# Performance work log

Measured on AMD Instinct MI355X. Metric: run time of the kernel, lower is better.

## Reference

```python
import jax, jax.numpy as jnp
import numpy as np

N = 50000        # nodes
E = 1600000      # edges
D_IN = 128       # input feature size
H = 4            # attention heads
C = 16           # hidden_size1 (per-head out channels)
HC = H * C       # 64
HS2 = 64         # hidden_size2
EDGE_DIM = 4
EPS = 1e-5


def setup_inputs() -> dict:
    key = jax.random.key(0)
    ks = jax.random.split(key, 64)
    inp = {}
    inp["data_x"] = jax.random.normal(ks[0], (N, D_IN), jnp.float32)
    inp["data_edge_index"] = jax.random.randint(ks[1], (2, E), 0, N)
    inp["data_edge_attr"] = jax.random.normal(ks[2], (E, EDGE_DIM), jnp.float32)
    i = 3
    s = 0.1
    for l, din in enumerate([D_IN, HC]):
        inp[f"Wl{l}"] = jax.random.normal(ks[i], (din, HC), jnp.float32) * s; i += 1
        inp[f"bl{l}"] = jnp.zeros((HC,), jnp.float32)
        inp[f"Wr{l}"] = jax.random.normal(ks[i], (din, HC), jnp.float32) * s; i += 1
        inp[f"br{l}"] = jnp.zeros((HC,), jnp.float32)
        inp[f"We{l}"] = jax.random.normal(ks[i], (EDGE_DIM, HC), jnp.float32) * s; i += 1
        inp[f"att{l}"] = jax.random.normal(ks[i], (H, C), jnp.float32) * s; i += 1
        inp[f"bias{l}"] = jnp.zeros((HC,), jnp.float32)
        inp[f"g{l}"] = jnp.ones((HC,), jnp.float32)
        inp[f"be{l}"] = jnp.zeros((HC,), jnp.float32)
    inp["W1"] = jax.random.normal(ks[i], (HC, HS2), jnp.float32) * s; i += 1
    inp["b1"] = jnp.zeros((HS2,), jnp.float32)
    inp["gf"] = jnp.ones((HS2,), jnp.float32)
    inp["bf"] = jnp.zeros((HS2,), jnp.float32)
    inp["W2"] = jax.random.normal(ks[i], (HS2, 1), jnp.float32) * s; i += 1
    inp["b2"] = jnp.zeros((1,), jnp.float32)
    return inp


def batch_norm(x, g, b):
    mu = x.mean(0)
    var = x.var(0)  # biased variance, matching torch BN normalization
    return (x - mu) * jax.lax.rsqrt(var + EPS) * g + b


def gatv2_layer(x, src, dst, eattr, Wl, bl, Wr, br, We, att, bias):
    # GATv2Conv, add_self_loops=False, concat=True, negative_slope=0.2
    n = x.shape[0]
    xl = (x @ Wl + bl).reshape(n, H, C)   # source transform (x_j side)
    xr = (x @ Wr + br).reshape(n, H, C)   # destination transform (x_i side)
    e = (eattr @ We).reshape(-1, H, C)    # edge-feature transform
    m = xl[src] + xr[dst] + e             # [E,H,C]
    m = jnp.where(m > 0, m, 0.2 * m)      # LeakyReLU(0.2)
    a = jnp.einsum('ehc,hc->eh', m, att)  # attention logits [E,H]
    amax = jax.ops.segment_max(a, dst, num_segments=n)   # per-dst max
    a = jnp.exp(a - amax[dst])
    asum = jax.ops.segment_sum(a, dst, num_segments=n)
    alpha = a / (asum[dst] + 1e-16)       # per-destination softmax
    out = jax.ops.segment_sum(xl[src] * alpha[:, :, None], dst, num_segments=n)
    return out.reshape(n, HC) + bias


def reference(data_x, data_edge_index, data_edge_attr,
              Wl0, bl0, Wr0, br0, We0, att0, bias0, g0, be0,
              Wl1, bl1, Wr1, br1, We1, att1, bias1, g1, be1,
              W1, b1, gf, bf, W2, b2):
    src = data_edge_index[0]
    dst = data_edge_index[1]
    layers = [(Wl0, bl0, Wr0, br0, We0, att0, bias0, g0, be0),
              (Wl1, bl1, Wr1, br1, We1, att1, bias1, g1, be1)]
    x = data_x
    for (Wl, bl, Wr, br, We, att, bias, g, be) in layers:
        x = gatv2_layer(x, src, dst, data_edge_attr, Wl, bl, Wr, br, We, att, bias)
        x = jax.nn.elu(batch_norm(x, g, be))
    x = x @ W1 + b1
    x = jax.nn.elu(batch_norm(x, gf, bf))
    return 5.0 * jnp.tanh(x @ W2 + b2)
```

## Files before the change

### kernel.cpp

```cpp
#include <hip/hip_runtime.h>
#include <hip/hip_bf16.h>
#include <cmath>

#define HC 64
typedef __hip_bfloat16 bf16;
typedef unsigned int uint;
typedef float v4f __attribute__((ext_vector_type(4)));

__device__ __forceinline__ uint pack_bf2(float a, float b) {
    __hip_bfloat162 h = __float22bfloat162_rn(make_float2(a, b));
    return *reinterpret_cast<uint*>(&h);
}
__device__ __forceinline__ float bfl(uint u) { return __uint_as_float(u << 16); }
__device__ __forceinline__ float bfh(uint u) { return __uint_as_float(u & 0xffff0000u); }


__global__ __launch_bounds__(512) void bucket_hist_k(const int* __restrict__ dst,
                                                     int* __restrict__ bcnt, int E, int nbk) {
    __shared__ int lh[512];
    int t = threadIdx.x;
    for (int i = t; i < nbk; i += 512) lh[i] = 0;
    __syncthreads();
    int base = blockIdx.x * 8192;
#pragma unroll
    for (int k = 0; k < 16; ++k) {
        int e = base + k * 512 + t;
        if (e < E) atomicAdd(&lh[dst[e] >> 7], 1);
    }
    __syncthreads();
    for (int i = t; i < nbk; i += 512) if (lh[i]) atomicAdd(&bcnt[i], lh[i]);
}


__global__ __launch_bounds__(512) void bucket_scan_k(const int* __restrict__ bcnt,
                                                     int* __restrict__ bstart,
                                                     int* __restrict__ bcur, int nbk, int E) {
    __shared__ int tmp[512];
    int t = threadIdx.x;
    int v = (t < nbk) ? bcnt[t] : 0;
    tmp[t] = v;
    __syncthreads();
    for (int off = 1; off < 512; off <<= 1) {
        int a = (t >= off) ? tmp[t - off] : 0;
        __syncthreads();
        tmp[t] += a;
        __syncthreads();
    }
    if (t < nbk) { int ex = tmp[t] - v; bstart[t] = ex; bcur[t] = ex; }
    if (t == 0) bstart[nbk] = E;
}


__global__ __launch_bounds__(1024) void bucketA_k(
        const int* __restrict__ src, const int* __restrict__ dst,
        const float4* __restrict__ eattr, int* __restrict__ bcur,
        uint* __restrict__ tsd, uint2* __restrict__ tea, int E, int nbk) {
    __shared__ int lcnt[512];
    __shared__ int lbase[512];
    int t = threadIdx.x;
    for (int i = t; i < nbk; i += 1024) lcnt[i] = 0;
    __syncthreads();
    int base = blockIdx.x * 8192;
    int myb[8], mylp[8];
#pragma unroll
    for (int k = 0; k < 8; ++k) {
        int e = base + k * 1024 + t;
        if (e < E) {
            int b = dst[e] >> 7;
            myb[k] = b;
            mylp[k] = atomicAdd(&lcnt[b], 1);
        } else myb[k] = -1;
    }
    __syncthreads();
    for (int i = t; i < nbk; i += 1024) {
        int cc = lcnt[i];
        lbase[i] = cc ? atomicAdd(&bcur[i], cc) : 0;
    }
    __syncthreads();
#pragma unroll
    for (int k = 0; k < 8; ++k) {
        int e = base + k * 1024 + t;
        if (e >= E) continue;
        int pos = lbase[myb[k]] + mylp[k];
        int d = dst[e];
        tsd[pos] = (uint)src[e] | ((uint)(d & 127) << 25);
        float4 ea = eattr[e];
        tea[pos] = make_uint2(pack_bf2(ea.x, ea.y), pack_bf2(ea.z, ea.w));
    }
}


__global__ __launch_bounds__(256) void bucket_sort_k(
        const uint* __restrict__ tsd, const uint2* __restrict__ tea,
        const int* __restrict__ bstart,
        uint* __restrict__ spre_sorted, uint2* __restrict__ eat_sorted,
        int* __restrict__ row_start, int n) {
    __shared__ int cnt[128], pfx[128], cur[128];
    int b = blockIdx.x, t = threadIdx.x;
    int i0 = bstart[b], i1 = bstart[b + 1];
    int node0 = b << 7;
    if (t < 128) cnt[t] = 0;
    __syncthreads();
    for (int i = i0 + t; i < i1; i += 256) atomicAdd(&cnt[tsd[i] >> 25], 1);
    __syncthreads();
    if (t < 128) pfx[t] = cnt[t];
    __syncthreads();
    for (int off = 1; off < 128; off <<= 1) {
        int a = (t < 128 && t >= off) ? pfx[t - off] : 0;
        __syncthreads();
        if (t < 128) pfx[t] += a;
        __syncthreads();
    }
    if (t < 128) {
        int ex = pfx[t] - cnt[t];
        cur[t] = ex;
        if (node0 + t <= n) row_start[node0 + t] = i0 + ex;
    }
    __syncthreads();
    for (int i = i0 + t; i < i1; i += 256) {
        uint u = tsd[i];
        int dl = (int)(u >> 25);
        int pos = i0 + atomicAdd(&cur[dl], 1);
        spre_sorted[pos] = (u & 0x1FFFFFFu) << 7;
        eat_sorted[pos] = tea[i];
    }
}


__global__ __launch_bounds__(256) void lin128_k(
        const float* __restrict__ x, int n,
        const float* __restrict__ Wl, const float* __restrict__ bl,
        const float* __restrict__ Wr, const float* __restrict__ br,
        bf16* __restrict__ xl, bf16* __restrict__ xr, int ngroups16) {
    __shared__ uint sWl2[64 * 64];
    __shared__ uint sWr2[64 * 64];
    __shared__ float sx[16 * 128];
    int t = threadIdx.x;
    for (int i = t; i < 64 * 64; i += 256) {
        int k2 = i >> 6, c = i & 63;
        sWl2[i] = pack_bf2(Wl[(2 * k2) * 64 + c], Wl[(2 * k2 + 1) * 64 + c]);
        sWr2[i] = pack_bf2(Wr[(2 * k2) * 64 + c], Wr[(2 * k2 + 1) * 64 + c]);
    }
    int c = t & 63, w = t >> 6;
    float blc = bl[c], brc = br[c];
    for (int gidx = blockIdx.x; gidx < ngroups16; gidx += gridDim.x) {
        int node0 = gidx * 16;
        __syncthreads();
        for (int i = t; i < 16 * 128; i += 256) {
            int r = node0 + (i >> 7);
            sx[i] = (r < n) ? x[(size_t)r * 128 + (i & 127)] : 0.f;
        }
        __syncthreads();
        float al0 = blc, al1 = blc, al2 = blc, al3 = blc;
        float ar0 = brc, ar1 = brc, ar2 = brc, ar3 = brc;
        const float* sx0 = sx + w * 4 * 128;
#pragma unroll 8
        for (int k2 = 0; k2 < 64; ++k2) {
            uint wlu = sWl2[k2 * 64 + c], wru = sWr2[k2 * 64 + c];
            float wlx = bfl(wlu), wly = bfh(wlu);
            float wrx = bfl(wru), wry = bfh(wru);
            float2 xa = *(const float2*)&sx0[k2 * 2];
            float2 xb = *(const float2*)&sx0[128 + k2 * 2];
            float2 xc = *(const float2*)&sx0[256 + k2 * 2];
            float2 xd = *(const float2*)&sx0[384 + k2 * 2];
            al0 = fmaf(xa.x, wlx, al0); al0 = fmaf(xa.y, wly, al0);
            ar0 = fmaf(xa.x, wrx, ar0); ar0 = fmaf(xa.y, wry, ar0);
            al1 = fmaf(xb.x, wlx, al1); al1 = fmaf(xb.y, wly, al1);
            ar1 = fmaf(xb.x, wrx, ar1); ar1 = fmaf(xb.y, wry, ar1);
            al2 = fmaf(xc.x, wlx, al2); al2 = fmaf(xc.y, wly, al2);
            ar2 = fmaf(xc.x, wrx, ar2); ar2 = fmaf(xc.y, wry, ar2);
            al3 = fmaf(xd.x, wlx, al3); al3 = fmaf(xd.y, wly, al3);
            ar3 = fmaf(xd.x, wrx, ar3); ar3 = fmaf(xd.y, wry, ar3);
        }
        int nb_ = node0 + w * 4;
        if (nb_ + 0 < n) { xl[(size_t)(nb_ + 0) * 64 + c] = __float2bfloat16(al0); xr[(size_t)(nb_ + 0) * 64 + c] = __float2bfloat16(ar0); }
        if (nb_ + 1 < n) { xl[(size_t)(nb_ + 1) * 64 + c] = __float2bfloat16(al1); xr[(size_t)(nb_ + 1) * 64 + c] = __float2bfloat16(ar1); }
        if (nb_ + 2 < n) { xl[(size_t)(nb_ + 2) * 64 + c] = __float2bfloat16(al2); xr[(size_t)(nb_ + 2) * 64 + c] = __float2bfloat16(ar2); }
        if (nb_ + 3 < n) { xl[(size_t)(nb_ + 3) * 64 + c] = __float2bfloat16(al3); xr[(size_t)(nb_ + 3) * 64 + c] = __float2bfloat16(ar3); }
    }
}


__global__ __launch_bounds__(256) void lin64bn_k(
        const float* __restrict__ x, int n,
        const float* __restrict__ sums, const float* __restrict__ sqs,
        const float* __restrict__ g, const float* __restrict__ be,
        const float* __restrict__ Wl, const float* __restrict__ bl,
        const float* __restrict__ Wr, const float* __restrict__ br,
        bf16* __restrict__ xl, bf16* __restrict__ xr, int ngroups16) {
    __shared__ uint sWl2[32 * 64];
    __shared__ uint sWr2[32 * 64];
    __shared__ float sx[16 * 64];
    __shared__ float ssc[64], ssh[64];
    int t = threadIdx.x;
    if (t < 64) {
        float inv_n = 1.f / n;
        float mu = sums[t] * inv_n;
        float var = sqs[t] * inv_n - mu * mu;
        float sc = rsqrtf(var + 1e-5f) * g[t];
        ssc[t] = sc; ssh[t] = be[t] - mu * sc;
    }
    for (int i = t; i < 32 * 64; i += 256) {
        int k2 = i >> 6, c = i & 63;
        sWl2[i] = pack_bf2(Wl[(2 * k2) * 64 + c], Wl[(2 * k2 + 1) * 64 + c]);
        sWr2[i] = pack_bf2(Wr[(2 * k2) * 64 + c], Wr[(2 * k2 + 1) * 64 + c]);
    }
    int c = t & 63, w = t >> 6;
    float blc = bl[c], brc = br[c];
    for (int gidx = blockIdx.x; gidx < ngroups16; gidx += gridDim.x) {
        int node0 = gidx * 16;
        __syncthreads();
        for (int i = t; i < 16 * 64; i += 256) {
            int r = node0 + (i >> 6);
            float v = (r < n) ? x[(size_t)r * 64 + (i & 63)] : 0.f;
            v = v * ssc[i & 63] + ssh[i & 63];
            sx[i] = v > 0.f ? v : __expf(v) - 1.f;
        }
        __syncthreads();
        float al0 = blc, al1 = blc, al2 = blc, al3 = blc;
        float ar0 = brc, ar1 = brc, ar2 = brc, ar3 = brc;
        const float* sx0 = sx + w * 4 * 64;
#pragma unroll 8
        for (int k2 = 0; k2 < 32; ++k2) {
            uint wlu = sWl2[k2 * 64 + c], wru = sWr2[k2 * 64 + c];
            float wlx = bfl(wlu), wly = bfh(wlu);
            float wrx = bfl(wru), wry = bfh(wru);
            float2 xa = *(const float2*)&sx0[k2 * 2];
            float2 xb = *(const float2*)&sx0[64 + k2 * 2];
            float2 xc = *(const float2*)&sx0[128 + k2 * 2];
            float2 xd = *(const float2*)&sx0[192 + k2 * 2];
            al0 = fmaf(xa.x, wlx, al0); al0 = fmaf(xa.y, wly, al0);
            ar0 = fmaf(xa.x, wrx, ar0); ar0 = fmaf(xa.y, wry, ar0);
            al1 = fmaf(xb.x, wlx, al1); al1 = fmaf(xb.y, wly, al1);
            ar1 = fmaf(xb.x, wrx, ar1); ar1 = fmaf(xb.y, wry, ar1);
            al2 = fmaf(xc.x, wlx, al2); al2 = fmaf(xc.y, wly, al2);
            ar2 = fmaf(xc.x, wrx, ar2); ar2 = fmaf(xc.y, wry, ar2);
            al3 = fmaf(xd.x, wlx, al3); al3 = fmaf(xd.y, wly, al3);
            ar3 = fmaf(xd.x, wrx, ar3); ar3 = fmaf(xd.y, wry, ar3);
        }
        int nb_ = node0 + w * 4;
        if (nb_ + 0 < n) { xl[(size_t)(nb_ + 0) * 64 + c] = __float2bfloat16(al0); xr[(size_t)(nb_ + 0) * 64 + c] = __float2bfloat16(ar0); }
        if (nb_ + 1 < n) { xl[(size_t)(nb_ + 1) * 64 + c] = __float2bfloat16(al1); xr[(size_t)(nb_ + 1) * 64 + c] = __float2bfloat16(ar1); }
        if (nb_ + 2 < n) { xl[(size_t)(nb_ + 2) * 64 + c] = __float2bfloat16(al2); xr[(size_t)(nb_ + 2) * 64 + c] = __float2bfloat16(ar2); }
        if (nb_ + 3 < n) { xl[(size_t)(nb_ + 3) * 64 + c] = __float2bfloat16(al3); xr[(size_t)(nb_ + 3) * 64 + c] = __float2bfloat16(ar3); }
    }
}


__global__ __launch_bounds__(256) void gat_node_k(
        const bf16* __restrict__ xl, const bf16* __restrict__ xr,
        const float* __restrict__ We, const float* __restrict__ att,
        const int* __restrict__ row_start, const uint* __restrict__ spre,
        const uint2* __restrict__ eat,
        float* __restrict__ out, int n) {
    int t = threadIdx.x;
    int lane = t & 63;
    int quad = lane >> 4;
    int c4 = lane & 15;
    int node = blockIdx.x * 4 + (t >> 6);
    if (node >= n) return;
    int c0 = c4 << 2;
    v4f w0 = {We[c0], We[c0 + 1], We[c0 + 2], We[c0 + 3]};
    v4f w1 = {We[64 + c0], We[64 + c0 + 1], We[64 + c0 + 2], We[64 + c0 + 3]};
    v4f w2 = {We[128 + c0], We[128 + c0 + 1], We[128 + c0 + 2], We[128 + c0 + 3]};
    v4f w3 = {We[192 + c0], We[192 + c0 + 1], We[192 + c0 + 2], We[192 + c0 + 3]};
    v4f ratt = {att[c0] * 1.44269504f, att[c0 + 1] * 1.44269504f,
                att[c0 + 2] * 1.44269504f, att[c0 + 3] * 1.44269504f};
    const char* xlb = (const char*)xl;
    uint2 xru = *(const uint2*)((const char*)xr + ((size_t)node << 7) + ((uint)c0 << 1));
    v4f xrd = {bfl(xru.x), bfh(xru.x), bfl(xru.y), bfh(xru.y)};
    int rs = row_start[node], re = row_start[node + 1];
    v4f acc = {0.f, 0.f, 0.f, 0.f};
    float srun = 0.f;
    uint coff = (uint)c4 << 3;

#define PROC(EA, XU) { \
        v4f xv = {bfl((XU).x), bfh((XU).x), bfl((XU).y), bfh((XU).y)}; \
        v4f z = xv + xrd; \
        float e0 = bfl((EA).x), e1 = bfh((EA).x); \
        float e2 = bfl((EA).y), e3 = bfh((EA).y); \
        z += e0 * w0; z += e1 * w1; z += e2 * w2; z += e3 * w3; \
        z = __builtin_elementwise_max(z, 0.2f * z); \
        v4f zr = z * ratt; \
        float v = (zr.x + zr.y) + (zr.z + zr.w); \
        v += __shfl_xor(v, 1); v += __shfl_xor(v, 2); \
        float p = exp2f(v); \
        srun += p; \
        acc += p * xv; \
    }

    int i = rs;
    for (; i + 16 <= re; i += 16) {
        uint sp0 = spre[i + quad],      sp1 = spre[i + 4 + quad];
        uint sp2 = spre[i + 8 + quad],  sp3 = spre[i + 12 + quad];
        uint2 ea0 = eat[i + quad],      ea1 = eat[i + 4 + quad];
        uint2 ea2 = eat[i + 8 + quad],  ea3 = eat[i + 12 + quad];
        uint2 xu0 = *(const uint2*)(xlb + sp0 + coff);
        uint2 xu1 = *(const uint2*)(xlb + sp1 + coff);
        uint2 xu2 = *(const uint2*)(xlb + sp2 + coff);
        uint2 xu3 = *(const uint2*)(xlb + sp3 + coff);
        PROC(ea0, xu0);
        PROC(ea1, xu1);
        PROC(ea2, xu2);
        PROC(ea3, xu3);
    }
    for (; i + 8 <= re; i += 8) {
        uint spA = spre[i + quad], spB = spre[i + 4 + quad];
        uint2 eaA = eat[i + quad], eaB = eat[i + 4 + quad];
        uint2 xuA = *(const uint2*)(xlb + spA + coff);
        uint2 xuB = *(const uint2*)(xlb + spB + coff);
        PROC(eaA, xuA);
        PROC(eaB, xuB);
    }
    for (; i < re; i += 4) {
        int ei = i + quad;
        bool ok = ei < re;
        int eic = ok ? ei : i;
        uint sp = spre[eic];
        uint2 ea = eat[eic];
        uint2 xu = *(const uint2*)(xlb + sp + coff);
        v4f xv = {bfl(xu.x), bfh(xu.x), bfl(xu.y), bfh(xu.y)};
        v4f z = xv + xrd;
        float e0 = bfl(ea.x), e1 = bfh(ea.x);
        float e2 = bfl(ea.y), e3 = bfh(ea.y);
        z += e0 * w0; z += e1 * w1; z += e2 * w2; z += e3 * w3;
        z = __builtin_elementwise_max(z, 0.2f * z);
        v4f zr = z * ratt;
        float v = (zr.x + zr.y) + (zr.z + zr.w);
        v += __shfl_xor(v, 1); v += __shfl_xor(v, 2);
        float p = ok ? exp2f(v) : 0.f;
        srun += p;
        acc += p * xv;
    }
#undef PROC

    srun += __shfl_xor(srun, 16);  srun += __shfl_xor(srun, 32);
    acc.x += __shfl_xor(acc.x, 16); acc.x += __shfl_xor(acc.x, 32);
    acc.y += __shfl_xor(acc.y, 16); acc.y += __shfl_xor(acc.y, 32);
    acc.z += __shfl_xor(acc.z, 16); acc.z += __shfl_xor(acc.z, 32);
    acc.w += __shfl_xor(acc.w, 16); acc.w += __shfl_xor(acc.w, 32);
    if (quad == 0) {
        float inv = 1.f / (srun + 1e-16f);
        v4f o = acc * inv;
        *(v4f*)&out[((size_t)node << 6) + (uint)c0] = o;
    }
}


__global__ void bn_stats_k(const float* __restrict__ x, float* __restrict__ sums,
                           float* __restrict__ sqs, int n) {
    __shared__ float ls[256], lq[256];
    int t = threadIdx.x;
    int c = t & 63, sub = t >> 6;
    float s = 0.f, q = 0.f;
    for (int r = blockIdx.x * 4 + sub; r < n; r += gridDim.x * 4) {
        float v = x[(size_t)r * 64 + c];
        s += v;
        q = fmaf(v, v, q);
    }
    ls[t] = s; lq[t] = q;
    __syncthreads();
    if (t < 128) { ls[t] += ls[t + 128]; lq[t] += lq[t + 128]; }
    __syncthreads();
    if (t < 64) {
        atomicAdd(&sums[c], ls[t] + ls[t + 64]);
        atomicAdd(&sqs[c], lq[t] + lq[t + 64]);
    }
}


__global__ __launch_bounds__(256) void lin1_k(
        const float* __restrict__ x, int n,
        const float* __restrict__ sums, const float* __restrict__ sqs,
        const float* __restrict__ g, const float* __restrict__ be,
        const float* __restrict__ W, const float* __restrict__ b,
        float* __restrict__ y, float* __restrict__ sums_o, float* __restrict__ sqs_o,
        int ngroups16) {
    __shared__ uint sW2[32 * 64];
    __shared__ float sx[16 * 64];
    __shared__ float ssc[64], ssh[64];
    __shared__ float ls[256], lq[256];
    int t = threadIdx.x;
    if (t < 64) {
        float inv_n = 1.f / n;
        float mu = sums[t] * inv_n;
        float var = sqs[t] * inv_n - mu * mu;
        float sc = rsqrtf(var + 1e-5f) * g[t];
        ssc[t] = sc; ssh[t] = be[t] - mu * sc;
    }
    for (int i = t; i < 32 * 64; i += 256) {
        int k2 = i >> 6, c = i & 63;
        sW2[i] = pack_bf2(W[(2 * k2) * 64 + c], W[(2 * k2 + 1) * 64 + c]);
    }
    int c = t & 63, w = t >> 6;
    float bc = b[c];
    float s = 0.f, q = 0.f;
    for (int gidx = blockIdx.x; gidx < ngroups16; gidx += gridDim.x) {
        int node0 = gidx * 16;
        __syncthreads();
        for (int i = t; i < 16 * 64; i += 256) {
            int r = node0 + (i >> 6);
            float v = (r < n) ? x[(size_t)r * 64 + (i & 63)] : 0.f;
            v = v * ssc[i & 63] + ssh[i & 63];
            sx[i] = v > 0.f ? v : __expf(v) - 1.f;
        }
        __syncthreads();
        float a0 = bc, a1 = bc, a2 = bc, a3 = bc;
        const float* sx0 = sx + w * 4 * 64;
#pragma unroll 8
        for (int k2 = 0; k2 < 32; ++k2) {
            uint wu = sW2[k2 * 64 + c];
            float wx = bfl(wu), wy = bfh(wu);
            float2 xa = *(const float2*)&sx0[k2 * 2];
            float2 xb = *(const float2*)&sx0[64 + k2 * 2];
            float2 xc = *(const float2*)&sx0[128 + k2 * 2];
            float2 xd = *(const float2*)&sx0[192 + k2 * 2];
            a0 = fmaf(xa.x, wx, a0); a0 = fmaf(xa.y, wy, a0);
            a1 = fmaf(xb.x, wx, a1); a1 = fmaf(xb.y, wy, a1);
            a2 = fmaf(xc.x, wx, a2); a2 = fmaf(xc.y, wy, a2);
            a3 = fmaf(xd.x, wx, a3); a3 = fmaf(xd.y, wy, a3);
        }
        int nb_ = node0 + w * 4;
        if (nb_ + 0 < n) { y[(size_t)(nb_ + 0) * 64 + c] = a0; s += a0; q = fmaf(a0, a0, q); }
        if (nb_ + 1 < n) { y[(size_t)(nb_ + 1) * 64 + c] = a1; s += a1; q = fmaf(a1, a1, q); }
        if (nb_ + 2 < n) { y[(size_t)(nb_ + 2) * 64 + c] = a2; s += a2; q = fmaf(a2, a2, q); }
        if (nb_ + 3 < n) { y[(size_t)(nb_ + 3) * 64 + c] = a3; s += a3; q = fmaf(a3, a3, q); }
    }
    __syncthreads();
    ls[t] = s; lq[t] = q;
    __syncthreads();
    if (t < 64) {
        float ss = ls[t] + ls[t + 64] + ls[t + 128] + ls[t + 192];
        float qq = lq[t] + lq[t + 64] + lq[t + 128] + lq[t + 192];
        atomicAdd(&sums_o[t], ss);
        atomicAdd(&sqs_o[t], qq);
    }
}


__global__ void final_k(const float* __restrict__ z, int n,
                        const float* __restrict__ sums, const float* __restrict__ sqs,
                        const float* __restrict__ g, const float* __restrict__ be,
                        const float* __restrict__ W2, const float* __restrict__ b2,
                        float* __restrict__ out) {
    int t = blockIdx.x * blockDim.x + threadIdx.x;
    int node = t >> 6, c = t & 63;
    if (node >= n) return;
    float inv_n = 1.f / n;
    float mu = sums[c] * inv_n;
    float var = sqs[c] * inv_n - mu * mu;
    float scc = rsqrtf(var + 1e-5f) * g[c];
    float sh = be[c] - mu * scc;
    float v = z[(size_t)node * 64 + c] * scc + sh;
    v = v > 0.f ? v : __expf(v) - 1.f;
    v *= W2[c];
    v += __shfl_xor(v, 1);
    v += __shfl_xor(v, 2);
    v += __shfl_xor(v, 4);
    v += __shfl_xor(v, 8);
    v += __shfl_xor(v, 16);
    v += __shfl_xor(v, 32);
    if (c == 0) out[node] = 5.0f * tanhf(v + b2[0]);
}


extern "C" void kernel_launch(void* const* d_in, const int* in_sizes, int n_in,
                              void* d_out, int out_size, void* d_ws, size_t ws_size,
                              hipStream_t stream) {
    const float* x0    = (const float*)d_in[0];
    const int*   eidx  = (const int*)d_in[1];
    const float* eattr = (const float*)d_in[2];

    const float* Wl[2]; const float* bl[2]; const float* Wr[2]; const float* br[2];
    const float* We[2]; const float* att[2]; const float* g[2]; const float* be[2];
    for (int l = 0; l < 2; ++l) {
        int base = 3 + l * 9;
        Wl[l]  = (const float*)d_in[base + 0];
        bl[l]  = (const float*)d_in[base + 1];
        Wr[l]  = (const float*)d_in[base + 2];
        br[l]  = (const float*)d_in[base + 3];
        We[l]  = (const float*)d_in[base + 4];
        att[l] = (const float*)d_in[base + 5];
        g[l]   = (const float*)d_in[base + 7];
        be[l]  = (const float*)d_in[base + 8];
    }
    const float* W1 = (const float*)d_in[21];
    const float* b1 = (const float*)d_in[22];
    const float* gf = (const float*)d_in[23];
    const float* bf = (const float*)d_in[24];
    const float* W2 = (const float*)d_in[25];
    const float* b2 = (const float*)d_in[26];

    const int N = in_sizes[0] / 128;
    const int E = in_sizes[1] / 2;
    const int* src = eidx;
    const int* dst = eidx + E;
    const int nbk = (N + 127) >> 7;

    float* ws = (float*)d_ws;
    size_t o = 0;
    float* regionA = ws + o; o += (size_t)2 * N * HC;
    uint2* tea = (uint2*)regionA;
    uint*  tsd = (uint*)(regionA + (size_t)2 * E);
    float* h0  = regionA;
    float* h1  = regionA + (size_t)N * HC;
    uint2* eat_sorted = (uint2*)(ws + o); o += (size_t)E * 2;
    uint*  spre_sorted = (uint*)(ws + o);  o += (size_t)E;
    bf16*  xl  = (bf16*)(ws + o);  o += (size_t)N * 32;
    bf16*  xr  = (bf16*)(ws + o);  o += (size_t)N * 32;
    int*   row_start = (int*)(ws + o); o += (size_t)N + 1;
    int*   bcnt   = (int*)(ws + o); o += 512;
    float* stats  = ws + o; o += 6 * HC;
    int*   bstart = (int*)(ws + o); o += 513;
    int*   bcur   = (int*)(ws + o); o += 512;
    float* s0 = stats,        *q0 = stats + 64;
    float* s1 = stats + 128,  *q1 = stats + 192;
    float* sf = stats + 256,  *qf = stats + 320;

    const int ngroups4  = (N + 3) / 4;
    const int ngroups16 = (N + 15) / 16;
    const int EB = (E + 8191) / 8192;
    const int lin_grid = ngroups16 < 1024 ? ngroups16 : 1024;

    hipMemsetAsync(bcnt, 0, (512 + 6 * HC) * 4, stream);

    bucket_hist_k<<<EB, 512, 0, stream>>>(dst, bcnt, E, nbk);
    bucket_scan_k<<<1, 512, 0, stream>>>(bcnt, bstart, bcur, nbk, E);
    bucketA_k<<<EB, 1024, 0, stream>>>(src, dst, (const float4*)eattr, bcur, tsd, tea, E, nbk);
    bucket_sort_k<<<nbk, 256, 0, stream>>>(tsd, tea, bstart, spre_sorted, eat_sorted,
                                           row_start, N);

    lin128_k<<<lin_grid, 256, 0, stream>>>(x0, N, Wl[0], bl[0], Wr[0], br[0], xl, xr, ngroups16);
    gat_node_k<<<ngroups4, 256, 0, stream>>>(xl, xr, We[0], att[0], row_start,
                                             spre_sorted, eat_sorted, h0, N);
    bn_stats_k<<<256, 256, 0, stream>>>(h0, s0, q0, N);

    lin64bn_k<<<lin_grid, 256, 0, stream>>>(h0, N, s0, q0, g[0], be[0],
                                            Wl[1], bl[1], Wr[1], br[1], xl, xr, ngroups16);
    gat_node_k<<<ngroups4, 256, 0, stream>>>(xl, xr, We[1], att[1], row_start,
                                             spre_sorted, eat_sorted, h1, N);
    bn_stats_k<<<256, 256, 0, stream>>>(h1, s1, q1, N);

    float* y = h0;
    lin1_k<<<lin_grid, 256, 0, stream>>>(h1, N, s1, q1, g[1], be[1], W1, b1, y, sf, qf, ngroups16);
    final_k<<<(int)(((size_t)N * 64 + 255) / 256), 256, 0, stream>>>(
        y, N, sf, qf, gf, bf, W2, b2, (float*)d_out);
}
```

Before: 362.0 us.

## Replace global atomic bucket offsets with per-block histogram and serial scan

The histogram kernel now writes a per-block, per-bucket count matrix instead of accumulating atomically into global bucket counts. A single-block scan computes each block's exclusive offset within every bucket, and the scatter kernel reads those offsets directly rather than claiming them with global atomics. This removes global atomic contention and makes the scatter order deterministic. The cost is a single-block scan in which each thread walks about 196 entries serially, twice, which may be slow.

```diff
diff --git a/kernel.cpp b/kernel.cpp
--- a/kernel.cpp
+++ b/kernel.cpp
@@ -15,30 +15,35 @@
 __device__ __forceinline__ float bfh(uint u) { return __uint_as_float(u & 0xffff0000u); }
 
 
-__global__ __launch_bounds__(512) void bucket_hist_k(const int* __restrict__ dst,
-                                                     int* __restrict__ bcnt, int E, int nbk) {
+__global__ __launch_bounds__(1024) void histA_k(const int* __restrict__ dst,
+                                                int* __restrict__ hist, int E, int nbk, int nblk) {
     __shared__ int lh[512];
     int t = threadIdx.x;
-    for (int i = t; i < nbk; i += 512) lh[i] = 0;
+    for (int i = t; i < nbk; i += 1024) lh[i] = 0;
     __syncthreads();
     int base = blockIdx.x * 8192;
 #pragma unroll
-    for (int k = 0; k < 16; ++k) {
-        int e = base + k * 512 + t;
+    for (int k = 0; k < 8; ++k) {
+        int e = base + k * 1024 + t;
         if (e < E) atomicAdd(&lh[dst[e] >> 7], 1);
     }
     __syncthreads();
-    for (int i = t; i < nbk; i += 512) if (lh[i]) atomicAdd(&bcnt[i], lh[i]);
-}
-
-
-__global__ __launch_bounds__(512) void bucket_scan_k(const int* __restrict__ bcnt,
-                                                     int* __restrict__ bstart,
-                                                     int* __restrict__ bcur, int nbk, int E) {
+    for (int i = t; i < nbk; i += 1024) hist[(size_t)i * nblk + blockIdx.x] = lh[i];
+}
+
+
+__global__ __launch_bounds__(512) void scan2_k(int* __restrict__ hist, int* __restrict__ bstart,
+                                               int nbk, int nblk, int E) {
     __shared__ int tmp[512];
     int t = threadIdx.x;
-    int v = (t < nbk) ? bcnt[t] : 0;
-    tmp[t] = v;
+    int cnt = 0;
+    if (t < nbk) {
+        int* row = hist + (size_t)t * nblk;
+        int run = 0;
+        for (int b = 0; b < nblk; ++b) { int v = row[b]; row[b] = run; run += v; }
+        cnt = run;
+    }
+    tmp[t] = cnt;
     __syncthreads();
     for (int off = 1; off < 512; off <<= 1) {
         int a = (t >= off) ? tmp[t - off] : 0;
@@ -46,43 +51,45 @@
         tmp[t] += a;
         __syncthreads();
     }
-    if (t < nbk) { int ex = tmp[t] - v; bstart[t] = ex; bcur[t] = ex; }
+    int ex = tmp[t] - cnt;
+    if (t < nbk) {
+        bstart[t] = ex;
+        int* row = hist + (size_t)t * nblk;
+        for (int b = 0; b < nblk; ++b) row[b] += ex;
+    }
     if (t == 0) bstart[nbk] = E;
 }
 
 
-__global__ __launch_bounds__(1024) void bucketA_k(
+__global__ __launch_bounds__(1024) void bucketC_k(
         const int* __restrict__ src, const int* __restrict__ dst,
-        const float4* __restrict__ eattr, int* __restrict__ bcur,
-        uint* __restrict__ tsd, uint2* __restrict__ tea, int E, int nbk) {
+        const float4* __restrict__ eattr, const int* __restrict__ hist,
+        uint* __restrict__ tsd, uint2* __restrict__ tea, int E, int nbk, int nblk) {
     __shared__ int lcnt[512];
     __shared__ int lbase[512];
     int t = threadIdx.x;
     for (int i = t; i < nbk; i += 1024) lcnt[i] = 0;
     __syncthreads();
     int base = blockIdx.x * 8192;
-    int myb[8], mylp[8];
+    int myd[8], mylp[8];
 #pragma unroll
     for (int k = 0; k < 8; ++k) {
         int e = base + k * 1024 + t;
         if (e < E) {
-            int b = dst[e] >> 7;
-            myb[k] = b;
-            mylp[k] = atomicAdd(&lcnt[b], 1);
-        } else myb[k] = -1;
-    }
-    __syncthreads();
-    for (int i = t; i < nbk; i += 1024) {
-        int cc = lcnt[i];
-        lbase[i] = cc ? atomicAdd(&bcur[i], cc) : 0;
-    }
+            int d = dst[e];
+            myd[k] = d;
+            mylp[k] = atomicAdd(&lcnt[d >> 7], 1);
+        } else myd[k] = -1;
+    }
+    __syncthreads();
+    for (int i = t; i < nbk; i += 1024) lbase[i] = hist[(size_t)i * nblk + blockIdx.x];
     __syncthreads();
 #pragma unroll
     for (int k = 0; k < 8; ++k) {
         int e = base + k * 1024 + t;
         if (e >= E) continue;
-        int pos = lbase[myb[k]] + mylp[k];
-        int d = dst[e];
+        int d = myd[k];
+        int pos = lbase[d >> 7] + mylp[k];
         tsd[pos] = (uint)src[e] | ((uint)(d & 127) << 25);
         float4 ea = eattr[e];
         tea[pos] = make_uint2(pack_bf2(ea.x, ea.y), pack_bf2(ea.z, ea.w));
@@ -496,6 +503,7 @@
     const int* src = eidx;
     const int* dst = eidx + E;
     const int nbk = (N + 127) >> 7;
+    const int nblkA = (E + 8191) / 8192;
 
     float* ws = (float*)d_ws;
     size_t o = 0;
@@ -509,24 +517,23 @@
     bf16*  xl  = (bf16*)(ws + o);  o += (size_t)N * 32;
     bf16*  xr  = (bf16*)(ws + o);  o += (size_t)N * 32;
     int*   row_start = (int*)(ws + o); o += (size_t)N + 1;
-    int*   bcnt   = (int*)(ws + o); o += 512;
+    int*   hist   = (int*)(ws + o); o += (size_t)nbk * nblkA + 64;
     float* stats  = ws + o; o += 6 * HC;
     int*   bstart = (int*)(ws + o); o += 513;
-    int*   bcur   = (int*)(ws + o); o += 512;
     float* s0 = stats,        *q0 = stats + 64;
     float* s1 = stats + 128,  *q1 = stats + 192;
     float* sf = stats + 256,  *qf = stats + 320;
 
     const int ngroups4  = (N + 3) / 4;
     const int ngroups16 = (N + 15) / 16;
-    const int EB = (E + 8191) / 8192;
     const int lin_grid = ngroups16 < 1024 ? ngroups16 : 1024;
 
-    hipMemsetAsync(bcnt, 0, (512 + 6 * HC) * 4, stream);
-
-    bucket_hist_k<<<EB, 512, 0, stream>>>(dst, bcnt, E, nbk);
-    bucket_scan_k<<<1, 512, 0, stream>>>(bcnt, bstart, bcur, nbk, E);
-    bucketA_k<<<EB, 1024, 0, stream>>>(src, dst, (const float4*)eattr, bcur, tsd, tea, E, nbk);
+    hipMemsetAsync(stats, 0, 6 * HC * 4, stream);
+
+    histA_k<<<nblkA, 1024, 0, stream>>>(dst, hist, E, nbk, nblkA);
+    scan2_k<<<1, 512, 0, stream>>>(hist, bstart, nbk, nblkA, E);
+    bucketC_k<<<nblkA, 1024, 0, stream>>>(src, dst, (const float4*)eattr, hist, tsd, tea,
+                                          E, nbk, nblkA);
     bucket_sort_k<<<nbk, 256, 0, stream>>>(tsd, tea, bstart, spre_sorted, eat_sorted,
                                            row_start, N);
 
```

After: 510.4 us. 41.0% more time.
